# Performance work log

Hardware: AMD Instinct MI355X
Metric: run time of the kernel (lower is better)

## Reference

```python
import jax, jax.numpy as jnp
import numpy as np

HIDDEN = 640
NQ = 10      # query heads
NKV = 2      # kv heads
HD = HIDDEN // NQ   # 64
GROUPS = NQ // NKV  # 5
THETA = 500000.0
EPS = 1e-6


def rmsnorm(x, g):
    rms = jnp.sqrt(jnp.mean(x * x, axis=-1, keepdims=True) + EPS)
    return x / rms * g


def bitlinear(x, w, g):
    """RMSNorm + ternary weight / int8 activation fake-quant + GEMM + rescale."""
    x = rmsnorm(x, g)
    alpha = jnp.maximum(jnp.mean(jnp.abs(w)), 1e-10)
    w_q = jnp.clip(jnp.round(w / alpha), -1.0, 1.0)
    w_q = w + jax.lax.stop_gradient(w_q - w)            # STE
    gamma = jnp.maximum(jnp.max(jnp.abs(x), axis=-1, keepdims=True), 1e-10)
    x_q = jnp.clip(jnp.round(x * 127.0 / gamma), -128.0, 127.0)
    x_q = x + jax.lax.stop_gradient(x_q - x)            # STE
    return (x_q @ w_q.T) * (alpha * gamma / 127.0)


def rope_tables(L):
    # half-dim cos/sin tables [L, HD//2]; equivalent to the torch code's
    # repeat_interleave followed by [..., ::2] slicing.
    freqs = 1.0 / THETA ** (jnp.arange(0, HD, 2, dtype=jnp.float32) / HD)
    ang = jnp.arange(L, dtype=jnp.float32)[:, None] * freqs[None, :]
    return jnp.cos(ang), jnp.sin(ang)


def apply_rope(x, cos, sin):
    # x: [B,H,L,D]; cos/sin: [L,D/2] broadcast over B,H
    x1 = x[..., ::2]
    x2 = x[..., 1::2]
    o1 = x1 * cos - x2 * sin
    o2 = x2 * cos + x1 * sin
    return jnp.stack([o1, o2], axis=-1).reshape(x.shape)


def setup_inputs() -> dict:
    key = jax.random.key(0)
    ks = jax.random.split(key, 6)
    B, L = 32, 512
    x = jax.random.normal(ks[0], (B, L, HIDDEN), dtype=jnp.float32)
    s_h = 1.0 / np.sqrt(HIDDEN)
    q_w = jax.random.normal(ks[1], (NQ * HD, HIDDEN), dtype=jnp.float32) * s_h
    k_w = jax.random.normal(ks[2], (NKV * HD, HIDDEN), dtype=jnp.float32) * s_h
    v_w = jax.random.normal(ks[3], (NKV * HD, HIDDEN), dtype=jnp.float32) * s_h
    o_w = jax.random.normal(ks[4], (HIDDEN, NQ * HD), dtype=jnp.float32) * (1.0 / np.sqrt(NQ * HD))
    ones = jnp.ones((HIDDEN,), dtype=jnp.float32)
    return {
        "x": x,
        "norm_w": ones,
        "q_w": q_w, "q_g": ones,
        "k_w": k_w, "k_g": ones,
        "v_w": v_w, "v_g": ones,
        "o_w": o_w, "o_g": jnp.ones((NQ * HD,), dtype=jnp.float32),
    }


def reference(x, norm_w, q_w, q_g, k_w, k_g, v_w, v_g, o_w, o_g):
    B, L, _ = x.shape
    residual = x
    h = rmsnorm(x, norm_w)
    q = bitlinear(h, q_w, q_g).reshape(B, L, NQ, HD).transpose(0, 2, 1, 3)
    k = bitlinear(h, k_w, k_g).reshape(B, L, NKV, HD).transpose(0, 2, 1, 3)
    v = bitlinear(h, v_w, v_g).reshape(B, L, NKV, HD).transpose(0, 2, 1, 3)
    cos, sin = rope_tables(L)
    q = apply_rope(q, cos, sin)
    k = apply_rope(k, cos, sin)
    k = jnp.repeat(k, GROUPS, axis=1)   # [B,NQ,L,HD]
    v = jnp.repeat(v, GROUPS, axis=1)
    scale = 1.0 / np.sqrt(HD).astype(np.float32)
    attn = jnp.einsum("bhqd,bhkd->bhqk", q, k) * scale
    attn = jax.nn.softmax(attn, axis=-1)
    out = jnp.einsum("bhqk,bhkd->bhqd", attn, v)
    out = out.transpose(0, 2, 1, 3).reshape(B, L, NQ * HD)
    return bitlinear(out, o_w, o_g) + residual
```

## Files before the change

kernel.cpp:

```cpp
#include <hip/hip_runtime.h>
#include <math.h>
#include <stdint.h>

#define HIDDEN 640
#define NTOK   16384
#define LSEQ   512
#define BATCH  32
#define NQH    10
#define NKVH   2
#define HDIM   64
#define GROUPS 5

typedef int      int4v  __attribute__((ext_vector_type(4)));
typedef int      int16v __attribute__((ext_vector_type(16)));
typedef _Float16 f16x8  __attribute__((ext_vector_type(8)));
typedef _Float16 f16x2  __attribute__((ext_vector_type(2)));
typedef float    f32x4  __attribute__((ext_vector_type(4)));

__device__ __forceinline__ float wred_sum(float v){
  #pragma unroll
  for (int m=1;m<64;m<<=1) v += __shfl_xor(v,m);
  return v;
}
__device__ __forceinline__ float wred_max(float v){
  #pragma unroll
  for (int m=1;m<64;m<<=1) v = fmaxf(v,__shfl_xor(v,m));
  return v;
}
__device__ __forceinline__ f16x2 pkmax(f16x2 a, f16x2 b){
  f16x2 r;
  r.x = (a.x > b.x) ? a.x : b.x;
  r.y = (a.y > b.y) ? a.y : b.y;
  return r;
}
__device__ __forceinline__ f16x2 shflx(f16x2 v, int m){
  int t = __builtin_bit_cast(int, v);
  t = __shfl_xor(t, m);
  return __builtin_bit_cast(f16x2, t);
}

__device__ __forceinline__ int frag_flat(int m, int k){
  return (((m>>5)*20 + (k>>5))<<10) + (((((k>>4)&1)<<5) | (m&31))<<4) + (k&15);
}

__global__ __launch_bounds__(256) void absum4_kernel(
    const float* __restrict__ w0, const float* __restrict__ w1,
    const float* __restrict__ w2, const float* __restrict__ w3,
    float* __restrict__ sums){
  const float* w; int n;
  switch(blockIdx.y){
    case 0:  w=w0; n=640*640; break;
    case 1:  w=w1; n=128*640; break;
    case 2:  w=w2; n=128*640; break;
    default: w=w3; n=640*640; break;
  }
  __shared__ float red[256];
  int tid = threadIdx.x;
  float s = 0.f;
  for (int i = blockIdx.x*256 + tid; i < n; i += gridDim.x*256) s += fabsf(w[i]);
  red[tid] = s; __syncthreads();
  for (int off=128; off>0; off>>=1){ if (tid<off) red[tid]+=red[tid+off]; __syncthreads(); }
  if (tid==0) atomicAdd(&sums[blockIdx.y], red[0]);
}

__global__ __launch_bounds__(256) void wquant4_kernel(
    const float* __restrict__ w0, const float* __restrict__ w1,
    const float* __restrict__ w2, const float* __restrict__ w3,
    int8_t* __restrict__ o0, int8_t* __restrict__ o1,
    int8_t* __restrict__ o2, int8_t* __restrict__ o3,
    const float* __restrict__ sums){
  const float* w; int8_t* o; int n;
  switch(blockIdx.y){
    case 0:  w=w0; o=o0; n=640*640; break;
    case 1:  w=w1; o=o1; n=128*640; break;
    case 2:  w=w2; o=o2; n=128*640; break;
    default: w=w3; o=o3; n=640*640; break;
  }
  float alpha = fmaxf(sums[blockIdx.y]/(float)n, 1e-10f);
  float inva  = 1.0f/alpha;
  int i = blockIdx.x*256 + threadIdx.x;
  if (i < n){
    float t = rintf(w[i]*inva);
    t = fminf(1.f, fmaxf(-1.f, t));
    int nr = i/640;
    int kc = i - nr*640;
    o[frag_flat(nr, kc)] = (int8_t)t;
  }
}

__global__ __launch_bounds__(256) void token_prep_kernel(
    const float* __restrict__ x, const float* __restrict__ nw,
    const float* __restrict__ qg, const float* __restrict__ kg, const float* __restrict__ vg,
    int8_t* __restrict__ xqq, int8_t* __restrict__ xqk, int8_t* __restrict__ xqv,
    float* __restrict__ gq, float* __restrict__ gk, float* __restrict__ gv){
  int lane = threadIdx.x & 63;
  int m = blockIdx.x*4 + (threadIdx.x>>6);
  const float* xr = x + (size_t)m*HIDDEN;
  int abase = ((m>>5)*20480) + ((m&31)<<4)
            + ((lane>>5)<<10) + (((lane>>4)&1)<<9) + (lane&15);
  float xv[10], h[10];
  float ss = 0.f;
  #pragma unroll
  for (int j=0;j<10;j++){ float t = xr[lane + 64*j]; xv[j]=t; ss += t*t; }
  float inv1 = 1.0f/sqrtf(wred_sum(ss)*(1.0f/HIDDEN) + 1e-6f);
  float ss2 = 0.f;
  #pragma unroll
  for (int j=0;j<10;j++){ float t = xv[j]*inv1*nw[lane+64*j]; h[j]=t; ss2 += t*t; }
  float inv2 = 1.0f/sqrtf(wred_sum(ss2)*(1.0f/HIDDEN) + 1e-6f);

  const float* gs[3] = {qg, kg, vg};
  int8_t* outs[3] = {xqq, xqk, xqv};
  float* gams[3] = {gq, gk, gv};
  #pragma unroll
  for (int s=0;s<3;s++){
    const float* g = gs[s];
    float t[10], amax = 0.f;
    #pragma unroll
    for (int j=0;j<10;j++){ float v = h[j]*inv2*g[lane+64*j]; t[j]=v; amax = fmaxf(amax, fabsf(v)); }
    float gamma = fmaxf(wred_max(amax), 1e-10f);
    float sc = 127.0f/gamma;
    int8_t* dst = outs[s] + abase;
    #pragma unroll
    for (int j=0;j<10;j++){
      float v = rintf(t[j]*sc);
      v = fminf(127.f, fmaxf(-128.f, v));
      dst[j*2048] = (int8_t)v;
    }
    if (lane==0) gams[s][m] = gamma;
  }
}

__global__ __launch_bounds__(256) void o_prep_kernel(const _Float16* __restrict__ ao,
    const float* __restrict__ og, int8_t* __restrict__ xqo, float* __restrict__ go){
  int lane = threadIdx.x & 63;
  int m = blockIdx.x*4 + (threadIdx.x>>6);
  const _Float16* xr = ao + (size_t)m*HIDDEN;
  int abase = ((m>>5)*20480) + ((m&31)<<4)
            + ((lane>>5)<<10) + (((lane>>4)&1)<<9) + (lane&15);
  float xv[10];
  float ss = 0.f;
  #pragma unroll
  for (int j=0;j<10;j++){ float t = (float)xr[lane + 64*j]; xv[j]=t; ss += t*t; }
  float inv = 1.0f/sqrtf(wred_sum(ss)*(1.0f/HIDDEN) + 1e-6f);
  float t[10], amax = 0.f;
  #pragma unroll
  for (int j=0;j<10;j++){ float v = xv[j]*inv*og[lane+64*j]; t[j]=v; amax = fmaxf(amax, fabsf(v)); }
  float gamma = fmaxf(wred_max(amax), 1e-10f);
  float sc = 127.0f/gamma;
  int8_t* dst = xqo + abase;
  #pragma unroll
  for (int j=0;j<10;j++){
    float v = rintf(t[j]*sc);
    v = fminf(127.f, fmaxf(-128.f, v));
    dst[j*2048] = (int8_t)v;
  }
  if (lane==0) go[m] = gamma;
}

__device__ __forceinline__ void gemm_core(
    const int8_t* __restrict__ xq, const int8_t* __restrict__ wqf,
    int m0, int n0, int lane, int16v& acc0, int16v& acc1){
  const int8_t* a0 = xq  + (size_t)(m0>>5)*20480 + (lane<<4);
  const int8_t* b0 = wqf + (size_t)(n0>>5)*20480 + (lane<<4);
  const int8_t* b1 = b0 + 20480;
  #pragma unroll
  for (int kb=0; kb<20; kb++){
    int4v a  = *(const int4v*)(a0 + (kb<<10));
    int4v v0 = *(const int4v*)(b0 + (kb<<10));
    int4v v1 = *(const int4v*)(b1 + (kb<<10));
    acc0 = __builtin_amdgcn_mfma_i32_32x32x32_i8(a, v0, acc0, 0, 0, 0);
    acc1 = __builtin_amdgcn_mfma_i32_32x32x32_i8(a, v1, acc1, 0, 0, 0);
  }
}

__global__ __launch_bounds__(256) void qkv_gemm_kernel(
    const int8_t* __restrict__ xq_q, const float* __restrict__ g_q, const int8_t* __restrict__ wq_q,
    const int8_t* __restrict__ xq_k, const float* __restrict__ g_k, const int8_t* __restrict__ wq_k,
    const int8_t* __restrict__ xq_v, const float* __restrict__ g_v, const int8_t* __restrict__ wq_v,
    const float* __restrict__ sums,
    _Float16* __restrict__ qbuf, _Float16* __restrict__ kbuf, _Float16* __restrict__ vbuf){
  __shared__ _Float16 Tr[4][64][40];
  int bx = blockIdx.x;
  const int8_t *xq, *wq; const float* gam; _Float16* outh;
  int n0, aidx, nheads, mode; float inv_nw, vscale;
  if (bx < 10){ xq=xq_q; wq=wq_q; gam=g_q; outh=qbuf; n0=bx*64;      aidx=0; inv_nw=1.0f/409600.f; nheads=NQH;  mode=1; vscale=0.18033688011110918f; }
  else if (bx < 12){ xq=xq_k; wq=wq_k; gam=g_k; outh=kbuf; n0=(bx-10)*64; aidx=1; inv_nw=1.0f/81920.f; nheads=NKVH; mode=1; vscale=1.0f; }
  else { xq=xq_v; wq=wq_v; gam=g_v; outh=vbuf; n0=(bx-12)*64; aidx=2; inv_nw=1.0f/81920.f; nheads=NKVH; mode=2; vscale=1.0f; }

  int lane = threadIdx.x & 63;
  int w    = threadIdx.x >> 6;
  int m0   = blockIdx.y*128 + w*32;
  int half = lane >> 5, lan5 = lane & 31;

  int16v acc0 = {0}, acc1 = {0};
  gemm_core(xq, wq, m0, n0, lane, acc0, acc1);

  float alpha = fmaxf(sums[aidx]*inv_nw, 1e-10f);
  float fr0 = 0.f, fr1 = 0.f;
  if (mode == 1){
    int d0 = (lan5) & ~1;
    int d1 = (32 + lan5) & ~1;
    fr0 = __expf(-(float)d0*(1.0f/64.0f)*13.122363377404328f);
    fr1 = __expf(-(float)d1*(1.0f/64.0f)*13.122363377404328f);
  }

  #pragma unroll
  for (int reg=0; reg<16; reg++){
    int ml = (reg&3) + 8*(reg>>2) + 4*half;
    int m = m0 + ml;
    float sc = alpha*gam[m]*(1.0f/127.0f);
    float v0 = (float)acc0[reg]*sc;
    float v1 = (float)acc1[reg]*sc;
    if (mode == 1){
      int b = m >> 9, l = m & 511;
      int head = n0 >> 6;
      float p0 = __shfl_xor(v0, 1);
      float p1 = __shfl_xor(v1, 1);
      float sn0, cs0, sn1, cs1;
      __sincosf((float)l*fr0, &sn0, &cs0);
      __sincosf((float)l*fr1, &sn1, &cs1);
      if (lane & 1){ v0 = v0*cs0 + p0*sn0;  v1 = v1*cs1 + p1*sn1; }
      else         { v0 = v0*cs0 - p0*sn0;  v1 = v1*cs1 - p1*sn1; }
      _Float16* dst = outh + ((((size_t)b*nheads + head)*LSEQ + l)<<6);
      dst[lan5]      = (_Float16)(v0*vscale);
      dst[32 + lan5] = (_Float16)(v1*vscale);
    } else {
      Tr[w][lan5][ml]      = (_Float16)v0;
      Tr[w][32 + lan5][ml] = (_Float16)v1;
    }
  }
  if (mode == 2){
    int b = m0 >> 9, l0 = m0 & 511;
    int head = n0 >> 6;
    f16x8 r0 = *(const f16x8*)&Tr[w][lane][0];
    f16x8 r1 = *(const f16x8*)&Tr[w][lane][8];
    f16x8 r2 = *(const f16x8*)&Tr[w][lane][16];
    f16x8 r3 = *(const f16x8*)&Tr[w][lane][24];
    _Float16* dst = outh + (((size_t)b*nheads + head)*HDIM + lane)*LSEQ + l0;
    ((f16x8*)dst)[0] = r0;
    ((f16x8*)dst)[1] = r1;
    ((f16x8*)dst)[2] = r2;
    ((f16x8*)dst)[3] = r3;
  }
}

__global__ __launch_bounds__(256) void out_gemm_kernel(
    const int8_t* __restrict__ xq, const float* __restrict__ gam,
    const int8_t* __restrict__ wq, const float* __restrict__ sums,
    const float* __restrict__ resid, float* __restrict__ outf){
  int lane = threadIdx.x & 63;
  int w    = threadIdx.x >> 6;
  int m0   = blockIdx.y*128 + w*32;
  int n0   = blockIdx.x*64;
  int half = lane >> 5, lan5 = lane & 31;

  int16v acc0 = {0}, acc1 = {0};
  gemm_core(xq, wq, m0, n0, lane, acc0, acc1);

  float alpha = fmaxf(sums[3]*(1.0f/409600.f), 1e-10f);
  #pragma unroll
  for (int reg=0; reg<16; reg++){
    int m = m0 + (reg&3) + 8*(reg>>2) + 4*half;
    float sc = alpha*gam[m]*(1.0f/127.0f);
    size_t ofs = (size_t)m*HIDDEN;
    outf[ofs + n0 + lan5]      = (float)acc0[reg]*sc + resid[ofs + n0 + lan5];
    outf[ofs + n0 + 32 + lan5] = (float)acc1[reg]*sc + resid[ofs + n0 + 32 + lan5];
  }
}

__device__ __forceinline__ int kv_addr(int row, int chunk){
  return (row<<6) + (((chunk ^ (row&7)))<<3);
}

__device__ __forceinline__ void softmax_update(
    f32x4* S, float* m_i, float* l_i, f32x4* O,
    _Float16 (*PsRow)[72], int quad, int c){
  float mxr[4], psr[4];
  #pragma unroll
  for (int r=0;r<4;r++)
    mxr[r] = fmaxf(fmaxf(S[0][r],S[1][r]), fmaxf(S[2][r],S[3][r]));
  f16x2 a01 = {(_Float16)mxr[0], (_Float16)mxr[1]};
  f16x2 a23 = {(_Float16)mxr[2], (_Float16)mxr[3]};
  #pragma unroll
  for (int mm=1; mm<16; mm<<=1){
    a01 = pkmax(a01, shflx(a01, mm));
    a23 = pkmax(a23, shflx(a23, mm));
  }
  float mn[4] = {(float)a01.x, (float)a01.y, (float)a23.x, (float)a23.y};
  #pragma unroll
  for (int r=0;r<4;r++){
    float mnew = fmaxf(m_i[r], mn[r]);
    float af = exp2f(m_i[r] - mnew);
    m_i[r] = mnew;
    float ps = 0.f;
    #pragma unroll
    for (int nt=0;nt<4;nt++){
      float p = exp2f(S[nt][r] - mnew);
      ps += p;
      PsRow[(quad<<2)+r][(nt<<4)+c] = (_Float16)p;
    }
    psr[r] = ps;
    l_i[r] *= af;
    O[0][r]*=af; O[1][r]*=af; O[2][r]*=af; O[3][r]*=af;
  }
  f16x2 s01 = {(_Float16)psr[0], (_Float16)psr[1]};
  f16x2 s23 = {(_Float16)psr[2], (_Float16)psr[3]};
  #pragma unroll
  for (int mm=1; mm<16; mm<<=1){
    s01 = s01 + shflx(s01, mm);
    s23 = s23 + shflx(s23, mm);
  }
  l_i[0] += (float)s01.x; l_i[1] += (float)s01.y;
  l_i[2] += (float)s23.x; l_i[3] += (float)s23.y;
}

__global__ __launch_bounds__(256,2) void attn_mfma_kernel(
    const _Float16* __restrict__ q, const _Float16* __restrict__ k,
    const _Float16* __restrict__ vt, _Float16* __restrict__ o){
  __shared__ _Float16 Ks[2][64*64];
  __shared__ _Float16 Vs[2][64*64];
  __shared__ _Float16 Ps[4][32][72];
  int tid  = threadIdx.x;
  int wv   = tid >> 6, lane = tid & 63;
  int quad = lane >> 4, c = lane & 15;
  int h = blockIdx.y, b = blockIdx.z;
  int hk = h / GROUPS;
  int qrow0 = blockIdx.x*128 + wv*32;

  const _Float16* qb = q + ((size_t)((b*NQH+h)*LSEQ) + qrow0 + c)*HDIM + quad*8;
  f16x8 qa0 = *(const f16x8*)qb;
  f16x8 qa1 = *(const f16x8*)(qb + 32);
  f16x8 qb0 = *(const f16x8*)(qb + 16*HDIM);
  f16x8 qb1 = *(const f16x8*)(qb + 16*HDIM + 32);

  const _Float16* kbase = k  + (size_t)((b*NKVH+hk)*LSEQ)*HDIM;
  const _Float16* vbase = vt + (size_t)((b*NKVH+hk)*HDIM)*LSEQ;

  int srow = tid >> 3, schunk = tid & 7;
  const _Float16* kg0 = kbase + (size_t)srow*HDIM      + schunk*8;
  const _Float16* kg1 = kbase + (size_t)(srow+32)*HDIM + schunk*8;
  const _Float16* vg0 = vbase + (size_t)srow*LSEQ      + schunk*8;
  const _Float16* vg1 = vbase + (size_t)(srow+32)*LSEQ + schunk*8;
  int ka0 = kv_addr(srow,    schunk);
  int ka1 = kv_addr(srow+32, schunk);

  {
    f16x8 t0 = *(const f16x8*)kg0;
    f16x8 t1 = *(const f16x8*)kg1;
    f16x8 t2 = *(const f16x8*)vg0;
    f16x8 t3 = *(const f16x8*)vg1;
    *(f16x8*)&Ks[0][ka0] = t0;
    *(f16x8*)&Ks[0][ka1] = t1;
    *(f16x8*)&Vs[0][ka0] = t2;
    *(f16x8*)&Vs[0][ka1] = t3;
  }

  f32x4 O0[4] = {{0,0,0,0},{0,0,0,0},{0,0,0,0},{0,0,0,0}};
  f32x4 O1[4] = {{0,0,0,0},{0,0,0,0},{0,0,0,0},{0,0,0,0}};
  float m0_[4] = {-INFINITY,-INFINITY,-INFINITY,-INFINITY};
  float m1_[4] = {-INFINITY,-INFINITY,-INFINITY,-INFINITY};
  float l0_[4] = {0,0,0,0}, l1_[4] = {0,0,0,0};
  f16x8 pk0, pk1, pv0, pv1;

  for (int kt=0; kt<8; kt++){
    __syncthreads();
    int cur = kt & 1, nxt = cur ^ 1;
    if (kt < 7){
      pk0 = *(const f16x8*)(kg0 + (size_t)(kt+1)*64*HDIM);
      pk1 = *(const f16x8*)(kg1 + (size_t)(kt+1)*64*HDIM);
      pv0 = *(const f16x8*)(vg0 + (kt+1)*64);
      pv1 = *(const f16x8*)(vg1 + (kt+1)*64);
    }
    f32x4 S0[4], S1[4];
    #pragma unroll
    for (int nt=0; nt<4; nt++){
      int row = (nt<<4) + c;
      f16x8 kf0 = *(const f16x8*)&Ks[cur][kv_addr(row, quad)];
      f16x8 kf1 = *(const f16x8*)&Ks[cur][kv_addr(row, quad+4)];
      f32x4 s = {0,0,0,0};
      s = __builtin_amdgcn_mfma_f32_16x16x32_f16(qa0, kf0, s, 0,0,0);
      s = __builtin_amdgcn_mfma_f32_16x16x32_f16(qa1, kf1, s, 0,0,0);
      S0[nt] = s;
      f32x4 s2 = {0,0,0,0};
      s2 = __builtin_amdgcn_mfma_f32_16x16x32_f16(qb0, kf0, s2, 0,0,0);
      s2 = __builtin_amdgcn_mfma_f32_16x16x32_f16(qb1, kf1, s2, 0,0,0);
      S1[nt] = s2;
    }
    softmax_update(S0, m0_, l0_, O0, (_Float16(*)[72])&Ps[wv][0],  quad, c);
    softmax_update(S1, m1_, l1_, O1, (_Float16(*)[72])&Ps[wv][16], quad, c);
    f16x8 p00 = *(const f16x8*)&Ps[wv][c][quad*8];
    f16x8 p01 = *(const f16x8*)&Ps[wv][c][quad*8 + 32];
    f16x8 p10 = *(const f16x8*)&Ps[wv][16+c][quad*8];
    f16x8 p11 = *(const f16x8*)&Ps[wv][16+c][quad*8 + 32];
    #pragma unroll
    for (int nt=0;nt<4;nt++){
      int row = (nt<<4) + c;
      f16x8 vf0 = *(const f16x8*)&Vs[cur][kv_addr(row, quad)];
      f16x8 vf1 = *(const f16x8*)&Vs[cur][kv_addr(row, quad+4)];
      O0[nt] = __builtin_amdgcn_mfma_f32_16x16x32_f16(p00, vf0, O0[nt], 0,0,0);
      O0[nt] = __builtin_amdgcn_mfma_f32_16x16x32_f16(p01, vf1, O0[nt], 0,0,0);
      O1[nt] = __builtin_amdgcn_mfma_f32_16x16x32_f16(p10, vf0, O1[nt], 0,0,0);
      O1[nt] = __builtin_amdgcn_mfma_f32_16x16x32_f16(p11, vf1, O1[nt], 0,0,0);
    }
    if (kt < 7){
      *(f16x8*)&Ks[nxt][ka0] = pk0;
      *(f16x8*)&Ks[nxt][ka1] = pk1;
      *(f16x8*)&Vs[nxt][ka0] = pv0;
      *(f16x8*)&Vs[nxt][ka1] = pv1;
    }
  }
  #pragma unroll
  for (int r=0;r<4;r++){
    float invl0 = 1.0f/l0_[r];
    float invl1 = 1.0f/l1_[r];
    int m0 = (b<<9) + qrow0 + (quad<<2) + r;
    _Float16* d0 = o + (size_t)m0*HIDDEN + (h<<6);
    _Float16* d1 = o + (size_t)(m0+16)*HIDDEN + (h<<6);
    #pragma unroll
    for (int nt=0;nt<4;nt++){
      d0[(nt<<4)+c] = (_Float16)(O0[nt][r]*invl0);
      d1[(nt<<4)+c] = (_Float16)(O1[nt][r]*invl1);
    }
  }
}

extern "C" void kernel_launch(void* const* d_in, const int* in_sizes, int n_in,
                              void* d_out, int out_size, void* d_ws, size_t ws_size,
                              hipStream_t stream){
  (void)in_sizes; (void)n_in; (void)out_size; (void)ws_size;
  const float* x  = (const float*)d_in[0];
  const float* nw = (const float*)d_in[1];
  const float* qw = (const float*)d_in[2];
  const float* qg = (const float*)d_in[3];
  const float* kw = (const float*)d_in[4];
  const float* kg = (const float*)d_in[5];
  const float* vw = (const float*)d_in[6];
  const float* vg = (const float*)d_in[7];
  const float* ow = (const float*)d_in[8];
  const float* og = (const float*)d_in[9];
  float* out = (float*)d_out;

  char* base = (char*)d_ws;
  size_t off = 0;
  auto alloc = [&](size_t nbytes)->void*{
    off = (off + 255) & ~(size_t)255;
    void* p = base + off;
    off += nbytes;
    return p;
  };
  float*  sums = (float*) alloc(4*sizeof(float));
  int8_t* wq_q = (int8_t*)alloc(640*640);
  int8_t* wq_k = (int8_t*)alloc(128*640);
  int8_t* wq_v = (int8_t*)alloc(128*640);
  int8_t* wq_o = (int8_t*)alloc(640*640);
  int8_t* xq_q = (int8_t*)alloc((size_t)NTOK*HIDDEN);
  int8_t* xq_k = (int8_t*)alloc((size_t)NTOK*HIDDEN);
  int8_t* xq_v = (int8_t*)alloc((size_t)NTOK*HIDDEN);
  int8_t* xq_o = (int8_t*)alloc((size_t)NTOK*HIDDEN);
  float*  g_q  = (float*) alloc((size_t)NTOK*4);
  float*  g_k  = (float*) alloc((size_t)NTOK*4);
  float*  g_v  = (float*) alloc((size_t)NTOK*4);
  float*  g_o  = (float*) alloc((size_t)NTOK*4);
  _Float16* qbuf = (_Float16*)alloc((size_t)BATCH*NQH *LSEQ*HDIM*2);
  _Float16* kbuf = (_Float16*)alloc((size_t)BATCH*NKVH*LSEQ*HDIM*2);
  _Float16* vbuf = (_Float16*)alloc((size_t)BATCH*NKVH*LSEQ*HDIM*2);
  _Float16* abuf = (_Float16*)alloc((size_t)NTOK*HIDDEN*2);

  (void)hipMemsetAsync(sums, 0, 4*sizeof(float), stream);
  absum4_kernel<<<dim3(64,4),256,0,stream>>>(qw, kw, vw, ow, sums);
  wquant4_kernel<<<dim3(1600,4),256,0,stream>>>(qw, kw, vw, ow, wq_q, wq_k, wq_v, wq_o, sums);

  token_prep_kernel<<<NTOK/4,256,0,stream>>>(x, nw, qg, kg, vg, xq_q, xq_k, xq_v, g_q, g_k, g_v);

  qkv_gemm_kernel<<<dim3(14,128),256,0,stream>>>(xq_q, g_q, wq_q,
                                                 xq_k, g_k, wq_k,
                                                 xq_v, g_v, wq_v,
                                                 sums, qbuf, kbuf, vbuf);

  attn_mfma_kernel<<<dim3(4,NQH,BATCH),256,0,stream>>>(qbuf, kbuf, vbuf, abuf);

  o_prep_kernel<<<NTOK/4,256,0,stream>>>(abuf, og, xq_o, g_o);
  out_gemm_kernel<<<dim3(10,128),256,0,stream>>>(xq_o, g_o, wq_o, sums, x, out);
}
```

Before: 260.6 us.

## Keep attention probabilities in registers via transposed S and permlane swaps

Swaps the MFMA operand order so each lane holds one query row's scores across keys. Softmax row reductions then need only two cross-lane shuffles, and the P fragments are rearranged in registers with permlane swap instructions instead of a round trip through shared memory. It also adds a lazy rescale that skips rescaling O unless the running max grows by more than a threshold. Occupancy is raised to 3 blocks per SM. The lazy rescale and in-register P layout are easy places to introduce subtle correctness errors, and register pressure rises.

After: 238.5 us. 8.5% less time.

```diff
diff --git a/kernel.cpp b/kernel.cpp
--- a/kernel.cpp
+++ b/kernel.cpp
@@ -26,17 +26,6 @@
   #pragma unroll
   for (int m=1;m<64;m<<=1) v = fmaxf(v,__shfl_xor(v,m));
   return v;
-}
-__device__ __forceinline__ f16x2 pkmax(f16x2 a, f16x2 b){
-  f16x2 r;
-  r.x = (a.x > b.x) ? a.x : b.x;
-  r.y = (a.y > b.y) ? a.y : b.y;
-  return r;
-}
-__device__ __forceinline__ f16x2 shflx(f16x2 v, int m){
-  int t = __builtin_bit_cast(int, v);
-  t = __shfl_xor(t, m);
-  return __builtin_bit_cast(f16x2, t);
 }
 
 __device__ __forceinline__ int frag_flat(int m, int k){
@@ -272,60 +261,69 @@
   return (row<<6) + (((chunk ^ (row&7)))<<3);
 }
 
-__device__ __forceinline__ void softmax_update(
-    f32x4* S, float* m_i, float* l_i, f32x4* O,
-    _Float16 (*PsRow)[72], int quad, int c){
-  float mxr[4], psr[4];
-  #pragma unroll
-  for (int r=0;r<4;r++)
-    mxr[r] = fmaxf(fmaxf(S[0][r],S[1][r]), fmaxf(S[2][r],S[3][r]));
-  f16x2 a01 = {(_Float16)mxr[0], (_Float16)mxr[1]};
-  f16x2 a23 = {(_Float16)mxr[2], (_Float16)mxr[3]};
-  #pragma unroll
-  for (int mm=1; mm<16; mm<<=1){
-    a01 = pkmax(a01, shflx(a01, mm));
-    a23 = pkmax(a23, shflx(a23, mm));
-  }
-  float mn[4] = {(float)a01.x, (float)a01.y, (float)a23.x, (float)a23.y};
-  #pragma unroll
-  for (int r=0;r<4;r++){
-    float mnew = fmaxf(m_i[r], mn[r]);
-    float af = exp2f(m_i[r] - mnew);
-    m_i[r] = mnew;
-    float ps = 0.f;
-    #pragma unroll
-    for (int nt=0;nt<4;nt++){
-      float p = exp2f(S[nt][r] - mnew);
-      ps += p;
-      PsRow[(quad<<2)+r][(nt<<4)+c] = (_Float16)p;
-    }
-    psr[r] = ps;
-    l_i[r] *= af;
-    O[0][r]*=af; O[1][r]*=af; O[2][r]*=af; O[3][r]*=af;
-  }
-  f16x2 s01 = {(_Float16)psr[0], (_Float16)psr[1]};
-  f16x2 s23 = {(_Float16)psr[2], (_Float16)psr[3]};
-  #pragma unroll
-  for (int mm=1; mm<16; mm<<=1){
-    s01 = s01 + shflx(s01, mm);
-    s23 = s23 + shflx(s23, mm);
-  }
-  l_i[0] += (float)s01.x; l_i[1] += (float)s01.y;
-  l_i[2] += (float)s23.x; l_i[3] += (float)s23.y;
-}
-
-__global__ __launch_bounds__(256,2) void attn_mfma_kernel(
+__device__ __forceinline__ void softmax_half(
+    const f32x4* S, float& m, float& l, f32x4* O, int quad,
+    f16x8& pf0, f16x8& pf1){
+  float t0 = fmaxf(fmaxf(S[0][0],S[0][1]), fmaxf(S[0][2],S[0][3]));
+  float t1 = fmaxf(fmaxf(S[1][0],S[1][1]), fmaxf(S[1][2],S[1][3]));
+  float t2 = fmaxf(fmaxf(S[2][0],S[2][1]), fmaxf(S[2][2],S[2][3]));
+  float t3 = fmaxf(fmaxf(S[3][0],S[3][1]), fmaxf(S[3][2],S[3][3]));
+  float tmax = fmaxf(fmaxf(t0,t1), fmaxf(t2,t3));
+  tmax = fmaxf(tmax, __shfl_xor(tmax, 16));
+  tmax = fmaxf(tmax, __shfl_xor(tmax, 32));
+  if (__any(tmax > m + 8.0f)){
+    float mnew = fmaxf(m, tmax);
+    float af = exp2f(m - mnew);
+    m = mnew;
+    l *= af;
+    #pragma unroll
+    for (int r=0;r<4;r++){
+      float afr = __shfl(af, (quad<<2)+r);
+      O[0][r]*=afr; O[1][r]*=afr; O[2][r]*=afr; O[3][r]*=afr;
+    }
+  }
+  float ps = 0.f;
+  uint32_t W[4][2];
+  #pragma unroll
+  for (int nt=0;nt<4;nt++){
+    float p0 = exp2f(S[nt][0]-m);
+    float p1 = exp2f(S[nt][1]-m);
+    float p2 = exp2f(S[nt][2]-m);
+    float p3 = exp2f(S[nt][3]-m);
+    ps += (p0+p1)+(p2+p3);
+    f16x2 w0 = {(_Float16)p0, (_Float16)p1};
+    f16x2 w1 = {(_Float16)p2, (_Float16)p3};
+    W[nt][0] = __builtin_bit_cast(uint32_t, w0);
+    W[nt][1] = __builtin_bit_cast(uint32_t, w1);
+  }
+  ps += __shfl_xor(ps, 16);
+  ps += __shfl_xor(ps, 32);
+  l += ps;
+  #pragma unroll
+  for (int p=0;p<2;p++){
+    asm volatile("v_permlane32_swap_b32 %0, %1" : "+v"(W[0][p]), "+v"(W[1][p]));
+    asm volatile("v_permlane32_swap_b32 %0, %1" : "+v"(W[2][p]), "+v"(W[3][p]));
+    asm volatile("v_permlane16_swap_b32 %0, %1" : "+v"(W[0][p]), "+v"(W[1][p]));
+    asm volatile("v_permlane16_swap_b32 %0, %1" : "+v"(W[2][p]), "+v"(W[3][p]));
+  }
+  union { uint32_t u[4]; f16x8 v; } a, b;
+  a.u[0]=W[0][0]; a.u[1]=W[0][1]; a.u[2]=W[1][0]; a.u[3]=W[1][1];
+  b.u[0]=W[2][0]; b.u[1]=W[2][1]; b.u[2]=W[3][0]; b.u[3]=W[3][1];
+  pf0 = a.v; pf1 = b.v;
+}
+
+__global__ __launch_bounds__(256,3) void attn_mfma_kernel(
     const _Float16* __restrict__ q, const _Float16* __restrict__ k,
     const _Float16* __restrict__ vt, _Float16* __restrict__ o){
   __shared__ _Float16 Ks[2][64*64];
   __shared__ _Float16 Vs[2][64*64];
-  __shared__ _Float16 Ps[4][32][72];
   int tid  = threadIdx.x;
   int wv   = tid >> 6, lane = tid & 63;
   int quad = lane >> 4, c = lane & 15;
   int h = blockIdx.y, b = blockIdx.z;
   int hk = h / GROUPS;
   int qrow0 = blockIdx.x*128 + wv*32;
+  (void)wv;
 
   const _Float16* qb = q + ((size_t)((b*NQH+h)*LSEQ) + qrow0 + c)*HDIM + quad*8;
   f16x8 qa0 = *(const f16x8*)qb;
@@ -357,9 +355,8 @@
 
   f32x4 O0[4] = {{0,0,0,0},{0,0,0,0},{0,0,0,0},{0,0,0,0}};
   f32x4 O1[4] = {{0,0,0,0},{0,0,0,0},{0,0,0,0},{0,0,0,0}};
-  float m0_[4] = {-INFINITY,-INFINITY,-INFINITY,-INFINITY};
-  float m1_[4] = {-INFINITY,-INFINITY,-INFINITY,-INFINITY};
-  float l0_[4] = {0,0,0,0}, l1_[4] = {0,0,0,0};
+  float m0s = -INFINITY, m1s = -INFINITY;
+  float l0s = 0.f, l1s = 0.f;
   f16x8 pk0, pk1, pv0, pv1;
 
   for (int kt=0; kt<8; kt++){
@@ -378,29 +375,26 @@
       f16x8 kf0 = *(const f16x8*)&Ks[cur][kv_addr(row, quad)];
       f16x8 kf1 = *(const f16x8*)&Ks[cur][kv_addr(row, quad+4)];
       f32x4 s = {0,0,0,0};
-      s = __builtin_amdgcn_mfma_f32_16x16x32_f16(qa0, kf0, s, 0,0,0);
-      s = __builtin_amdgcn_mfma_f32_16x16x32_f16(qa1, kf1, s, 0,0,0);
+      s = __builtin_amdgcn_mfma_f32_16x16x32_f16(kf0, qa0, s, 0,0,0);
+      s = __builtin_amdgcn_mfma_f32_16x16x32_f16(kf1, qa1, s, 0,0,0);
       S0[nt] = s;
       f32x4 s2 = {0,0,0,0};
-      s2 = __builtin_amdgcn_mfma_f32_16x16x32_f16(qb0, kf0, s2, 0,0,0);
-      s2 = __builtin_amdgcn_mfma_f32_16x16x32_f16(qb1, kf1, s2, 0,0,0);
+      s2 = __builtin_amdgcn_mfma_f32_16x16x32_f16(kf0, qb0, s2, 0,0,0);
+      s2 = __builtin_amdgcn_mfma_f32_16x16x32_f16(kf1, qb1, s2, 0,0,0);
       S1[nt] = s2;
     }
-    softmax_update(S0, m0_, l0_, O0, (_Float16(*)[72])&Ps[wv][0],  quad, c);
-    softmax_update(S1, m1_, l1_, O1, (_Float16(*)[72])&Ps[wv][16], quad, c);
-    f16x8 p00 = *(const f16x8*)&Ps[wv][c][quad*8];
-    f16x8 p01 = *(const f16x8*)&Ps[wv][c][quad*8 + 32];
-    f16x8 p10 = *(const f16x8*)&Ps[wv][16+c][quad*8];
-    f16x8 p11 = *(const f16x8*)&Ps[wv][16+c][quad*8 + 32];
+    f16x8 pf00, pf01, pf10, pf11;
+    softmax_half(S0, m0s, l0s, O0, quad, pf00, pf01);
+    softmax_half(S1, m1s, l1s, O1, quad, pf10, pf11);
     #pragma unroll
     for (int nt=0;nt<4;nt++){
       int row = (nt<<4) + c;
       f16x8 vf0 = *(const f16x8*)&Vs[cur][kv_addr(row, quad)];
       f16x8 vf1 = *(const f16x8*)&Vs[cur][kv_addr(row, quad+4)];
-      O0[nt] = __builtin_amdgcn_mfma_f32_16x16x32_f16(p00, vf0, O0[nt], 0,0,0);
-      O0[nt] = __builtin_amdgcn_mfma_f32_16x16x32_f16(p01, vf1, O0[nt], 0,0,0);
-      O1[nt] = __builtin_amdgcn_mfma_f32_16x16x32_f16(p10, vf0, O1[nt], 0,0,0);
-      O1[nt] = __builtin_amdgcn_mfma_f32_16x16x32_f16(p11, vf1, O1[nt], 0,0,0);
+      O0[nt] = __builtin_amdgcn_mfma_f32_16x16x32_f16(pf00, vf0, O0[nt], 0,0,0);
+      O0[nt] = __builtin_amdgcn_mfma_f32_16x16x32_f16(pf01, vf1, O0[nt], 0,0,0);
+      O1[nt] = __builtin_amdgcn_mfma_f32_16x16x32_f16(pf10, vf0, O1[nt], 0,0,0);
+      O1[nt] = __builtin_amdgcn_mfma_f32_16x16x32_f16(pf11, vf1, O1[nt], 0,0,0);
     }
     if (kt < 7){
       *(f16x8*)&Ks[nxt][ka0] = pk0;
@@ -411,8 +405,8 @@
   }
   #pragma unroll
   for (int r=0;r<4;r++){
-    float invl0 = 1.0f/l0_[r];
-    float invl1 = 1.0f/l1_[r];
+    float invl0 = 1.0f/__shfl(l0s, (quad<<2)+r);
+    float invl1 = 1.0f/__shfl(l1s, (quad<<2)+r);
     int m0 = (b<<9) + qrow0 + (quad<<2) + r;
     _Float16* d0 = o + (size_t)m0*HIDDEN + (h<<6);
     _Float16* d1 = o + (size_t)(m0+16)*HIDDEN + (h<<6);
```
